# Optimization experiments

Hardware: AMD Instinct MI355X
Metric: run time of the kernel (lower is better)

Reference implementation:

```python
import jax, jax.numpy as jnp
import numpy as np

N, E = 100000, 1600000
IN_CH, OUT_CH = 50, 121


def setup_inputs() -> dict:
    key = jax.random.key(0)
    ks = jax.random.split(key, 7)
    x = jax.random.normal(ks[0], (N, IN_CH), dtype=jnp.float32)
    edge_index = jax.random.randint(ks[1], (2, E), 0, N, dtype=jnp.int64)
    # MLP params (torch Linear default init: U(-1/sqrt(fan_in), 1/sqrt(fan_in)))
    b1_bound = 1.0 / np.sqrt(IN_CH)
    b2_bound = 1.0 / np.sqrt(OUT_CH)
    W1 = jax.random.uniform(ks[2], (IN_CH, OUT_CH), jnp.float32, -b1_bound, b1_bound)
    b1 = jax.random.uniform(ks[3], (OUT_CH,), jnp.float32, -b1_bound, b1_bound)
    W2 = jax.random.uniform(ks[4], (OUT_CH, OUT_CH), jnp.float32, -b2_bound, b2_bound)
    b2 = jax.random.uniform(ks[5], (OUT_CH,), jnp.float32, -b2_bound, b2_bound)
    eps = jnp.zeros((1,), dtype=jnp.float32)
    return {"x": x, "edge_index": edge_index, "W1": W1, "b1": b1,
            "W2": W2, "b2": b2, "eps": eps}


def reference(x, edge_index, W1, b1, W2, b2, eps):
    row, col = edge_index[0], edge_index[1]
    x_i = x[row]                      # [E, in_ch] gather
    x_j = x[col]                      # [E, in_ch] gather
    h = (1.0 + eps) * x_i + x_j       # eps-weighted combine
    h = jax.nn.relu(h @ W1 + b1)      # [E, out_ch]
    return h @ W2 + b2                # [E, out_ch]
```

## Files before the change

### kernel.cpp

```cpp
#include <hip/hip_runtime.h>
#include <hip/hip_bf16.h>
#include <stdint.h>

#define IN_CH 50
#define OUT_CH 121
#define OUT_PAD 128
#define LDS_STRIDE 136

typedef __attribute__((ext_vector_type(8))) __bf16 bf16x8;
typedef __attribute__((ext_vector_type(8))) short short8;
typedef __attribute__((ext_vector_type(4))) float f32x4;

__device__ __forceinline__ unsigned short f2bf(float f) {
  union { float f; unsigned int u; } v; v.f = f;
  unsigned int u = v.u;
  unsigned int r = u + 0x7fffu + ((u >> 16) & 1u);
  return (unsigned short)(r >> 16);
}
__device__ __forceinline__ float bf2f(unsigned short b) {
  union { unsigned int u; float f; } v; v.u = ((unsigned int)b) << 16;
  return v.f;
}

__global__ __launch_bounds__(128) void node_mlp1(
    const float* __restrict__ x, const float* __restrict__ W1,
    unsigned short* __restrict__ y, int Nn) {
  __shared__ float xs[8 * IN_CH];
  int nb = blockIdx.x * 8;
  int tid = threadIdx.x;
  for (int i = tid; i < 8 * IN_CH; i += 128) {
    int node = nb + i / IN_CH;
    xs[i] = (node < Nn) ? x[(size_t)nb * IN_CH + i] : 0.f;
  }
  __syncthreads();
  int c = tid;
  float acc[8];
#pragma unroll
  for (int n = 0; n < 8; ++n) acc[n] = 0.f;
  if (c < OUT_CH) {
    for (int k = 0; k < IN_CH; ++k) {
      float w = W1[k * OUT_CH + c];
#pragma unroll
      for (int n = 0; n < 8; ++n) acc[n] += xs[n * IN_CH + k] * w;
    }
  }
#pragma unroll
  for (int n = 0; n < 8; ++n) {
    if (nb + n < Nn) {
      unsigned short v = (c < OUT_CH) ? f2bf(acc[n]) : (unsigned short)0;
      y[(size_t)(nb + n) * OUT_PAD + c] = v;
    }
  }
}

__global__ __launch_bounds__(256) void prep_w2(
    const float* __restrict__ W2, unsigned short* __restrict__ w2t) {
  int idx = blockIdx.x * 256 + threadIdx.x;
  int n = idx >> 7, k = idx & 127;
  float v = (n < OUT_CH && k < OUT_CH) ? W2[k * OUT_CH + n] : 0.f;
  w2t[idx] = f2bf(v);
}

__global__ __launch_bounds__(256, 3) void edge_mlp2(
    const unsigned short* __restrict__ y,
    const int* __restrict__ eidx,
    const uint4* __restrict__ w2t4,
    const float* __restrict__ b1,
    const float* __restrict__ b2,
    const float* __restrict__ eps,
    float* __restrict__ out,
    int E) {
  __shared__ __align__(16) unsigned short sW[128 * LDS_STRIDE];
  __shared__ __align__(16) unsigned short sH[64 * LDS_STRIDE];
  __shared__ float sB1[128];
  __shared__ float sB2[128];
  int tid = threadIdx.x;

  for (int c = tid; c < 2048; c += 256) {
    int n = c >> 4, k8 = (c & 15) << 3;
    *((uint4*)&sW[n * LDS_STRIDE + k8]) = w2t4[c];
  }
  if (tid < 128) {
    sB1[tid] = (tid < OUT_CH) ? b1[tid] : 0.f;
    sB2[tid] = (tid < OUT_CH) ? b2[tid] : 0.f;
  }
  __syncthreads();

  float one_eps = 1.0f + eps[0];

  {
    int el = tid >> 2;
    int part = tid & 3;
    int e = blockIdx.x * 64 + el;
    size_t r  = (size_t)(unsigned)eidx[e];
    size_t cc = (size_t)(unsigned)eidx[E + e];
    const uint4* yr = (const uint4*)(y + r * OUT_PAD + part * 32);
    const uint4* yc = (const uint4*)(y + cc * OUT_PAD + part * 32);
#pragma unroll
    for (int q = 0; q < 4; ++q) {
      uint4 a = yr[q];
      uint4 b = yc[q];
      unsigned int aw[4] = {a.x, a.y, a.z, a.w};
      unsigned int bw[4] = {b.x, b.y, b.z, b.w};
      unsigned int hw[4];
#pragma unroll
      for (int p = 0; p < 4; ++p) {
        int ch = part * 32 + q * 8 + p * 2;
        float v0 = one_eps * bf2f((unsigned short)(aw[p] & 0xffffu)) +
                   bf2f((unsigned short)(bw[p] & 0xffffu)) + sB1[ch];
        float v1 = one_eps * bf2f((unsigned short)(aw[p] >> 16)) +
                   bf2f((unsigned short)(bw[p] >> 16)) + sB1[ch + 1];
        v0 = fmaxf(v0, 0.f);
        v1 = fmaxf(v1, 0.f);
        hw[p] = (unsigned int)f2bf(v0) | ((unsigned int)f2bf(v1) << 16);
      }
      uint4 hv;
      hv.x = hw[0]; hv.y = hw[1]; hv.z = hw[2]; hv.w = hw[3];
      *((uint4*)&sH[el * LDS_STRIDE + part * 32 + q * 8]) = hv;
    }
  }
  __syncthreads();

  int lane = tid & 63;
  int wv = tid >> 6;
  int q = lane >> 4;
  int l15 = lane & 15;

  short8 afr[4];
#pragma unroll
  for (int ks = 0; ks < 4; ++ks)
    afr[ks] = *(const short8*)&sH[(wv * 16 + l15) * LDS_STRIDE + q * 8 + ks * 32];

  f32x4 acc[8];
#pragma unroll
  for (int nt = 0; nt < 8; ++nt) acc[nt] = (f32x4){0.f, 0.f, 0.f, 0.f};

#pragma unroll
  for (int nt = 0; nt < 8; ++nt) {
#pragma unroll
    for (int ks = 0; ks < 4; ++ks) {
      short8 bfr = *(const short8*)&sW[(nt * 16 + l15) * LDS_STRIDE + q * 8 + ks * 32];
      acc[nt] = __builtin_amdgcn_mfma_f32_16x16x32_bf16(
          __builtin_bit_cast(bf16x8, afr[ks]),
          __builtin_bit_cast(bf16x8, bfr), acc[nt], 0, 0, 0);
    }
  }

  __syncthreads();
  float* out_s = (float*)sW;
  int erow = wv * 16 + q * 4;
#pragma unroll
  for (int nt = 0; nt < 8; ++nt) {
    int n = nt * 16 + l15;
    if (n < OUT_CH) {
      float bb = sB2[n];
#pragma unroll
      for (int rr = 0; rr < 4; ++rr)
        out_s[(erow + rr) * OUT_CH + n] = acc[nt][rr] + bb;
    }
  }
  __syncthreads();
  size_t base = (size_t)blockIdx.x * 64 * OUT_CH;
  for (int i = tid; i < 64 * OUT_CH; i += 256)
    out[base + i] = out_s[i];
}

extern "C" void kernel_launch(void* const* d_in, const int* in_sizes, int n_in,
                              void* d_out, int out_size, void* d_ws, size_t ws_size,
                              hipStream_t stream) {
  const float* x      = (const float*)d_in[0];
  const int* ei       = (const int*)d_in[1];
  const float* W1     = (const float*)d_in[2];
  const float* b1     = (const float*)d_in[3];
  const float* W2     = (const float*)d_in[4];
  const float* b2     = (const float*)d_in[5];
  const float* eps    = (const float*)d_in[6];
  float* out          = (float*)d_out;

  int N = in_sizes[0] / IN_CH;
  int E = in_sizes[1] / 2;

  unsigned short* y   = (unsigned short*)d_ws;
  unsigned short* w2t = y + (size_t)N * OUT_PAD;

  node_mlp1<<<(N + 7) / 8, 128, 0, stream>>>(x, W1, y, N);
  prep_w2<<<64, 256, 0, stream>>>(W2, w2t);
  edge_mlp2<<<E / 64, 256, 0, stream>>>(y, ei, (const uint4*)w2t,
                                        b1, b2, eps, out, E);
}
```

Before: 945.7 us.

## Process 128 edges per block, gather directly into MFMA fragments, prefetch indices

Each block now handles 128 edges, two 16-row MFMA tiles per wave. This halves the number of per-block W2 loads into LDS and reuses each B fragment across two MMAs. The gathered node rows are combined straight into MFMA A-fragments in registers, removing the sH LDS staging and one barrier. Edge indices are loaded before the weight staging to overlap latency, and outputs use nontemporal stores. Register pressure rises substantially, which may cause spills or lower occupancy.

```diff
diff --git a/kernel.cpp b/kernel.cpp
--- a/kernel.cpp
+++ b/kernel.cpp
@@ -1,5 +1,4 @@
 #include <hip/hip_runtime.h>
-#include <hip/hip_bf16.h>
 #include <stdint.h>
 
 #define IN_CH 50
@@ -59,6 +58,26 @@
   int n = idx >> 7, k = idx & 127;
   float v = (n < OUT_CH && k < OUT_CH) ? W2[k * OUT_CH + n] : 0.f;
   w2t[idx] = f2bf(v);
+}
+
+__device__ __forceinline__ short8 combine8(const uint4& a, const uint4& b,
+                                           const f32x4& bia, const f32x4& bib,
+                                           float one_eps) {
+  float bv[8] = {bia[0], bia[1], bia[2], bia[3], bib[0], bib[1], bib[2], bib[3]};
+  unsigned int aw[4] = {a.x, a.y, a.z, a.w};
+  unsigned int bw[4] = {b.x, b.y, b.z, b.w};
+  union { short8 v; unsigned int w[4]; } u;
+#pragma unroll
+  for (int p = 0; p < 4; ++p) {
+    float v0 = one_eps * bf2f((unsigned short)(aw[p] & 0xffffu)) +
+               bf2f((unsigned short)(bw[p] & 0xffffu)) + bv[2 * p];
+    float v1 = one_eps * bf2f((unsigned short)(aw[p] >> 16)) +
+               bf2f((unsigned short)(bw[p] >> 16)) + bv[2 * p + 1];
+    v0 = fmaxf(v0, 0.f);
+    v1 = fmaxf(v1, 0.f);
+    u.w[p] = (unsigned int)f2bf(v0) | ((unsigned int)f2bf(v1) << 16);
+  }
+  return u.v;
 }
 
 __global__ __launch_bounds__(256, 3) void edge_mlp2(
@@ -71,98 +90,104 @@
     float* __restrict__ out,
     int E) {
   __shared__ __align__(16) unsigned short sW[128 * LDS_STRIDE];
-  __shared__ __align__(16) unsigned short sH[64 * LDS_STRIDE];
-  __shared__ float sB1[128];
+  __shared__ __align__(16) float sB1[128];
   __shared__ float sB2[128];
   int tid = threadIdx.x;
-
-  for (int c = tid; c < 2048; c += 256) {
-    int n = c >> 4, k8 = (c & 15) << 3;
-    *((uint4*)&sW[n * LDS_STRIDE + k8]) = w2t4[c];
-  }
-  if (tid < 128) {
-    sB1[tid] = (tid < OUT_CH) ? b1[tid] : 0.f;
-    sB2[tid] = (tid < OUT_CH) ? b2[tid] : 0.f;
-  }
-  __syncthreads();
-
-  float one_eps = 1.0f + eps[0];
-
-  {
-    int el = tid >> 2;
-    int part = tid & 3;
-    int e = blockIdx.x * 64 + el;
-    size_t r  = (size_t)(unsigned)eidx[e];
-    size_t cc = (size_t)(unsigned)eidx[E + e];
-    const uint4* yr = (const uint4*)(y + r * OUT_PAD + part * 32);
-    const uint4* yc = (const uint4*)(y + cc * OUT_PAD + part * 32);
-#pragma unroll
-    for (int q = 0; q < 4; ++q) {
-      uint4 a = yr[q];
-      uint4 b = yc[q];
-      unsigned int aw[4] = {a.x, a.y, a.z, a.w};
-      unsigned int bw[4] = {b.x, b.y, b.z, b.w};
-      unsigned int hw[4];
-#pragma unroll
-      for (int p = 0; p < 4; ++p) {
-        int ch = part * 32 + q * 8 + p * 2;
-        float v0 = one_eps * bf2f((unsigned short)(aw[p] & 0xffffu)) +
-                   bf2f((unsigned short)(bw[p] & 0xffffu)) + sB1[ch];
-        float v1 = one_eps * bf2f((unsigned short)(aw[p] >> 16)) +
-                   bf2f((unsigned short)(bw[p] >> 16)) + sB1[ch + 1];
-        v0 = fmaxf(v0, 0.f);
-        v1 = fmaxf(v1, 0.f);
-        hw[p] = (unsigned int)f2bf(v0) | ((unsigned int)f2bf(v1) << 16);
-      }
-      uint4 hv;
-      hv.x = hw[0]; hv.y = hw[1]; hv.z = hw[2]; hv.w = hw[3];
-      *((uint4*)&sH[el * LDS_STRIDE + part * 32 + q * 8]) = hv;
-    }
-  }
-  __syncthreads();
-
   int lane = tid & 63;
   int wv = tid >> 6;
   int q = lane >> 4;
   int l15 = lane & 15;
 
-  short8 afr[4];
-#pragma unroll
-  for (int ks = 0; ks < 4; ++ks)
-    afr[ks] = *(const short8*)&sH[(wv * 16 + l15) * LDS_STRIDE + q * 8 + ks * 32];
-
-  f32x4 acc[8];
-#pragma unroll
-  for (int nt = 0; nt < 8; ++nt) acc[nt] = (f32x4){0.f, 0.f, 0.f, 0.f};
+  int e0 = blockIdx.x * 128 + wv * 32 + l15;
+  int r0 = __builtin_nontemporal_load(&eidx[e0]);
+  int c0 = __builtin_nontemporal_load(&eidx[E + e0]);
+  int r1 = __builtin_nontemporal_load(&eidx[e0 + 16]);
+  int c1 = __builtin_nontemporal_load(&eidx[E + e0 + 16]);
+
+  for (int cc = tid; cc < 2048; cc += 256) {
+    int n = cc >> 4, k8 = (cc & 15) << 3;
+    *((uint4*)&sW[n * LDS_STRIDE + k8]) = w2t4[cc];
+  }
+  if (tid < 128) {
+    sB1[tid] = (tid < OUT_CH) ? b1[tid] : 0.f;
+    sB2[tid] = (tid < OUT_CH) ? b2[tid] : 0.f;
+  }
+  __syncthreads();
+
+  float one_eps = 1.0f + eps[0];
+
+  const uint4* yi0 = (const uint4*)(y + ((size_t)(unsigned)r0 << 7));
+  const uint4* yj0 = (const uint4*)(y + ((size_t)(unsigned)c0 << 7));
+  const uint4* yi1 = (const uint4*)(y + ((size_t)(unsigned)r1 << 7));
+  const uint4* yj1 = (const uint4*)(y + ((size_t)(unsigned)c1 << 7));
+  uint4 ga0[4], gb0[4], ga1[4], gb1[4];
+#pragma unroll
+  for (int ks = 0; ks < 4; ++ks) {
+    int seg = q + ks * 4;
+    ga0[ks] = yi0[seg]; gb0[ks] = yj0[seg];
+    ga1[ks] = yi1[seg]; gb1[ks] = yj1[seg];
+  }
+
+  short8 afr[2][4];
+#pragma unroll
+  for (int ks = 0; ks < 4; ++ks) {
+    f32x4 bia = *((const f32x4*)&sB1[q * 8 + ks * 32]);
+    f32x4 bib = *((const f32x4*)&sB1[q * 8 + ks * 32 + 4]);
+    afr[0][ks] = combine8(ga0[ks], gb0[ks], bia, bib, one_eps);
+    afr[1][ks] = combine8(ga1[ks], gb1[ks], bia, bib, one_eps);
+  }
+
+  f32x4 acc[2][8];
+#pragma unroll
+  for (int m = 0; m < 2; ++m)
+#pragma unroll
+    for (int nt = 0; nt < 8; ++nt) acc[m][nt] = (f32x4){0.f, 0.f, 0.f, 0.f};
 
 #pragma unroll
   for (int nt = 0; nt < 8; ++nt) {
+    short8 bfr[4];
+#pragma unroll
+    for (int ks = 0; ks < 4; ++ks)
+      bfr[ks] = *(const short8*)&sW[(nt * 16 + l15) * LDS_STRIDE + q * 8 + ks * 32];
 #pragma unroll
     for (int ks = 0; ks < 4; ++ks) {
-      short8 bfr = *(const short8*)&sW[(nt * 16 + l15) * LDS_STRIDE + q * 8 + ks * 32];
-      acc[nt] = __builtin_amdgcn_mfma_f32_16x16x32_bf16(
-          __builtin_bit_cast(bf16x8, afr[ks]),
-          __builtin_bit_cast(bf16x8, bfr), acc[nt], 0, 0, 0);
+      acc[0][nt] = __builtin_amdgcn_mfma_f32_16x16x32_bf16(
+          __builtin_bit_cast(bf16x8, afr[0][ks]),
+          __builtin_bit_cast(bf16x8, bfr[ks]), acc[0][nt], 0, 0, 0);
+      acc[1][nt] = __builtin_amdgcn_mfma_f32_16x16x32_bf16(
+          __builtin_bit_cast(bf16x8, afr[1][ks]),
+          __builtin_bit_cast(bf16x8, bfr[ks]), acc[1][nt], 0, 0, 0);
     }
   }
 
   __syncthreads();
+  float bb[8];
+#pragma unroll
+  for (int nt = 0; nt < 8; ++nt) bb[nt] = sB2[nt * 16 + l15];
+
   float* out_s = (float*)sW;
-  int erow = wv * 16 + q * 4;
-#pragma unroll
-  for (int nt = 0; nt < 8; ++nt) {
-    int n = nt * 16 + l15;
-    if (n < OUT_CH) {
-      float bb = sB2[n];
-#pragma unroll
-      for (int rr = 0; rr < 4; ++rr)
-        out_s[(erow + rr) * OUT_CH + n] = acc[nt][rr] + bb;
-    }
-  }
-  __syncthreads();
-  size_t base = (size_t)blockIdx.x * 64 * OUT_CH;
-  for (int i = tid; i < 64 * OUT_CH; i += 256)
-    out[base + i] = out_s[i];
+  size_t base = (size_t)blockIdx.x * 128 * OUT_CH;
+#pragma unroll
+  for (int m = 0; m < 2; ++m) {
+    if (m) __syncthreads();
+    int erow = wv * 16 + q * 4;
+#pragma unroll
+    for (int nt = 0; nt < 8; ++nt) {
+      int n = nt * 16 + l15;
+      if (n < OUT_CH) {
+#pragma unroll
+        for (int rr = 0; rr < 4; ++rr)
+          out_s[(erow + rr) * OUT_CH + n] = acc[m][nt][rr] + bb[nt];
+      }
+    }
+    __syncthreads();
+    for (int g = 0; g < 4; ++g) {
+      size_t dst = base + (size_t)((g * 32 + m * 16) * OUT_CH);
+      const float* src = out_s + g * 16 * OUT_CH;
+      for (int j = tid; j < 16 * OUT_CH; j += 256)
+        __builtin_nontemporal_store(src[j], &out[dst + j]);
+    }
+  }
 }
 
 extern "C" void kernel_launch(void* const* d_in, const int* in_sizes, int n_in,
@@ -185,6 +210,6 @@
 
   node_mlp1<<<(N + 7) / 8, 128, 0, stream>>>(x, W1, y, N);
   prep_w2<<<64, 256, 0, stream>>>(W2, w2t);
-  edge_mlp2<<<E / 64, 256, 0, stream>>>(y, ei, (const uint4*)w2t,
-                                        b1, b2, eps, out, E);
-}
+  edge_mlp2<<<E / 128, 256, 0, stream>>>(y, ei, (const uint4*)w2t,
+                                         b1, b2, eps, out, E);
+}
```

New measurement: 910.5 us. -3.7%, faster.
